# Kernel tuning notes

Hardware: AMD Instinct MI355X
Metric: run time of the kernel (lower is better)

The kernel has to match this reference:

```python
import jax, jax.numpy as jnp
import numpy as np

N_NODES = 100000
N_EDGES = 1600000
IN_DIM, HID_DIM, N_CLASSES = 128, 64, 40


def spmm(edge_row, edge_col, edge_val, dense):
    # sparse [N,N] @ dense [N,D] via gather + segment-sum over edges
    msgs = edge_val[:, None] * dense[edge_col]            # [E, D]
    return jax.ops.segment_sum(msgs, edge_row, num_segments=N_NODES)


def setup_inputs() -> dict:
    key = jax.random.key(0)
    ks = jax.random.split(key, 8)
    x = jax.random.normal(ks[0], (N_NODES, IN_DIM), dtype=jnp.float32)
    edge_row = jax.random.randint(ks[1], (N_EDGES,), 0, N_NODES, dtype=jnp.int32)
    edge_col = jax.random.randint(ks[2], (N_EDGES,), 0, N_NODES, dtype=jnp.int32)
    edge_val = jax.random.uniform(ks[3], (N_EDGES,), dtype=jnp.float32)
    s1 = 1.0 / np.sqrt(IN_DIM)
    s2 = 1.0 / np.sqrt(HID_DIM)
    W1 = jax.random.normal(ks[4], (IN_DIM, HID_DIM), dtype=jnp.float32) * s1
    b1 = jnp.zeros((HID_DIM,), dtype=jnp.float32)
    W2 = jax.random.normal(ks[5], (HID_DIM, HID_DIM), dtype=jnp.float32) * s2
    b2 = jnp.zeros((HID_DIM,), dtype=jnp.float32)
    Wc = jax.random.normal(ks[6], (HID_DIM, N_CLASSES), dtype=jnp.float32) * s2
    bc = jnp.zeros((N_CLASSES,), dtype=jnp.float32)
    return {"x": x, "edge_row": edge_row, "edge_col": edge_col, "edge_val": edge_val,
            "W1": W1, "b1": b1, "W2": W2, "b2": b2, "Wc": Wc, "bc": bc}


def reference(x, edge_row, edge_col, edge_val, W1, b1, W2, b2, Wc, bc):
    # GCN layer 1: support = xW+b, aggregate, relu  (dropout off in eval)
    h = jax.nn.relu(spmm(edge_row, edge_col, edge_val, x @ W1 + b1))
    # GCN layer 2
    h = spmm(edge_row, edge_col, edge_val, h @ W2 + b2)
    # node classifier + log-softmax
    logits = h @ Wc + bc
    return jax.nn.log_softmax(logits, axis=-1)
```

## Files before the change

### kernel.cpp

```cpp
#include <hip/hip_runtime.h>

#define N_NODES   100000
#define N_EDGES   1600000
#define IN_DIM    128
#define HID_DIM   64
#define N_CLASSES 40

#define NBUCK 782
#define BCAP  2816
#define EPB   6400
#define PBLK  1024
#define G1BLK 1563

typedef __attribute__((ext_vector_type(8))) short bf16x8;
typedef __attribute__((ext_vector_type(4))) float f32x4;

__device__ inline short f2bf(float f) {
    unsigned u = __float_as_uint(f);
    unsigned r = (u + 0x7FFFu + ((u >> 16) & 1u)) >> 16;
    return (short)r;
}
__device__ inline float bflo(unsigned w) { return __uint_as_float(w << 16); }
__device__ inline float bfhi(unsigned w) { return __uint_as_float(w & 0xFFFF0000u); }
__device__ inline float upval(unsigned w) { return __uint_as_float((w >> 17) << 16); }

__global__ __launch_bounds__(256) void prep_weights(const float* __restrict__ W1,
                                                    const float* __restrict__ W2,
                                                    const float* __restrict__ Wc,
                                                    const float* __restrict__ b2,
                                                    short* __restrict__ W1t,
                                                    short* __restrict__ Mt,
                                                    float* __restrict__ bv,
                                                    int* __restrict__ bcnt) {
    for (int i = blockIdx.x * 256 + threadIdx.x; i < IN_DIM * HID_DIM; i += gridDim.x * 256) {
        int n = i >> 7, k = i & 127;
        W1t[i] = f2bf(W1[k * HID_DIM + n]);
    }
    if (blockIdx.x == 7) {
        for (int i = threadIdx.x; i < NBUCK; i += 256) bcnt[i] = 0;
    }
    if (blockIdx.x == 0) {
        for (int idx = threadIdx.x; idx < HID_DIM * HID_DIM; idx += 256) {
            int n = idx >> 6, i = idx & 63;
            float acc = 0.f;
            if (n < N_CLASSES)
                for (int j = 0; j < HID_DIM; ++j)
                    acc = fmaf(W2[i * HID_DIM + j], Wc[j * N_CLASSES + n], acc);
            Mt[n * HID_DIM + i] = f2bf(acc);
        }
        for (int n = threadIdx.x; n < N_CLASSES; n += 256) {
            float acc = 0.f;
            for (int j = 0; j < HID_DIM; ++j)
                acc = fmaf(b2[j], Wc[j * N_CLASSES + n], acc);
            bv[n] = acc;
        }
    }
}

__global__ __launch_bounds__(PBLK) void part_a(const int* __restrict__ erow,
                                               const int* __restrict__ ecol,
                                               const float* __restrict__ eval,
                                               int* __restrict__ bcnt,
                                               int2* __restrict__ tmp) {
    __shared__ int2 pay[EPB];
    __shared__ int hist[NBUCK], lbase[NBUCK], cur[NBUCK], dofs[NBUCK], scan[NBUCK];
    int e0 = blockIdx.x * EPB;
    int tid = threadIdx.x;
    for (int i = tid; i < NBUCK; i += PBLK) { hist[i] = 0; cur[i] = 0; }
    __syncthreads();
    for (int i = tid; i < EPB; i += PBLK)
        atomicAdd(&hist[erow[e0 + i] >> 7], 1);
    __syncthreads();
    for (int i = tid; i < NBUCK; i += PBLK) {
        int n = hist[i];
        dofs[i] = i * BCAP + (n ? atomicAdd(&bcnt[i], n) : 0);
        scan[i] = n;
    }
    __syncthreads();
    for (int off = 1; off < NBUCK; off <<= 1) {
        int t = 0;
        if (tid < NBUCK && tid >= off) t = scan[tid - off];
        __syncthreads();
        if (tid < NBUCK) scan[tid] += t;
        __syncthreads();
    }
    if (tid < NBUCK) {
        lbase[tid] = scan[tid] - hist[tid];
        dofs[tid] -= lbase[tid];
    }
    __syncthreads();
    for (int i = tid; i < EPB; i += PBLK) {
        int e = e0 + i;
        int r = erow[e];
        int b = r >> 7;
        int p = lbase[b] + atomicAdd(&cur[b], 1);
        unsigned u = __float_as_uint(eval[e]);
        unsigned vb = ((u + 0x7FFFu + ((u >> 16) & 1u)) >> 16) & 0x7FFFu;
        pay[p] = make_int2(((r & 127) << 17) | ecol[e], (int)((vb << 10) | (unsigned)b));
    }
    __syncthreads();
    for (int p = tid; p < EPB; p += PBLK) {
        int2 v = pay[p];
        int b = (unsigned)v.y & 1023u;
        int dest = dofs[b] + p;
        if (dest < (b + 1) * BCAP)
            tmp[dest] = v;
    }
}

__global__ __launch_bounds__(256) void part_b_gemm1(const int* __restrict__ bcnt,
                                                    const int2* __restrict__ tmp,
                                                    unsigned* __restrict__ tmp2,
                                                    int2* __restrict__ rowmeta,
                                                    const float* __restrict__ x,
                                                    const short* __restrict__ W1t,
                                                    const float* __restrict__ b1,
                                                    unsigned short* __restrict__ outH) {
    __shared__ int2 ein[BCAP];
    __shared__ unsigned eout[BCAP];
    __shared__ int hist[128], pad[128], basep[128], cur[128], scan[128];
    if (blockIdx.x < NBUCK) {
        int b = blockIdx.x;
        int nb = bcnt[b]; if (nb > BCAP) nb = BCAP;
        for (int i = threadIdx.x; i < nb; i += 256) ein[i] = tmp[(size_t)b * BCAP + i];
        if (threadIdx.x < 128) { hist[threadIdx.x] = 0; cur[threadIdx.x] = 0; }
        __syncthreads();
        for (int i = threadIdx.x; i < nb; i += 256)
            atomicAdd(&hist[(ein[i].x >> 17) & 127], 1);
        __syncthreads();
        if (threadIdx.x < 128) {
            pad[threadIdx.x] = (hist[threadIdx.x] + 3) & ~3;
            scan[threadIdx.x] = pad[threadIdx.x];
        }
        __syncthreads();
        for (int off = 1; off < 128; off <<= 1) {
            int t = 0;
            if (threadIdx.x < 128 && threadIdx.x >= off) t = scan[threadIdx.x - off];
            __syncthreads();
            if (threadIdx.x < 128) scan[threadIdx.x] += t;
            __syncthreads();
        }
        if (threadIdx.x < 128) basep[threadIdx.x] = scan[threadIdx.x] - pad[threadIdx.x];
        __syncthreads();
        int ntot = scan[127]; if (ntot > BCAP) ntot = BCAP;
        for (int i = threadIdx.x; i < nb; i += 256) {
            int lr = (ein[i].x >> 17) & 127;
            int p = basep[lr] + atomicAdd(&cur[lr], 1);
            if (p < BCAP) {
                unsigned vb = ((unsigned)ein[i].y >> 10) & 0x7FFFu;
                eout[p] = (vb << 17) | (unsigned)(ein[i].x & 0x1FFFF);
            }
        }
        __syncthreads();
        if (threadIdx.x < 128) {
            int pe = basep[threadIdx.x] + pad[threadIdx.x];
            for (int p = basep[threadIdx.x] + hist[threadIdx.x]; p < pe && p < BCAP; ++p)
                eout[p] = 0u;
        }
        __syncthreads();
        for (int i = threadIdx.x; i < ntot; i += 256) tmp2[(size_t)b * BCAP + i] = eout[i];
        if (threadIdx.x < 128) {
            int r = b * 128 + threadIdx.x;
            if (r < N_NODES)
                rowmeta[r] = make_int2(b * BCAP + basep[threadIdx.x], pad[threadIdx.x]);
        }
    } else {
        int gb = blockIdx.x - NBUCK;
        int wave = threadIdx.x >> 6;
        int lane = threadIdx.x & 63;
        int node0 = gb * 64 + wave * 16;
        if (node0 >= N_NODES) return;
        int m = lane & 15;
        int q = lane >> 4;
        const float* xrow = x + (size_t)(node0 + m) * IN_DIM;
        f32x4 acc0 = {0,0,0,0}, acc1 = {0,0,0,0}, acc2 = {0,0,0,0}, acc3 = {0,0,0,0};
#pragma unroll
        for (int kb = 0; kb < 4; ++kb) {
            int k0 = kb * 32 + q * 8;
            float4 a0 = *(const float4*)(xrow + k0);
            float4 a1 = *(const float4*)(xrow + k0 + 4);
            bf16x8 af;
            af[0]=f2bf(a0.x); af[1]=f2bf(a0.y); af[2]=f2bf(a0.z); af[3]=f2bf(a0.w);
            af[4]=f2bf(a1.x); af[5]=f2bf(a1.y); af[6]=f2bf(a1.z); af[7]=f2bf(a1.w);
            bf16x8 bf0 = *(const bf16x8*)(W1t + ( 0 + m) * IN_DIM + k0);
            bf16x8 bf1 = *(const bf16x8*)(W1t + (16 + m) * IN_DIM + k0);
            bf16x8 bf2 = *(const bf16x8*)(W1t + (32 + m) * IN_DIM + k0);
            bf16x8 bf3 = *(const bf16x8*)(W1t + (48 + m) * IN_DIM + k0);
            acc0 = __builtin_amdgcn_mfma_f32_16x16x32_bf16(af, bf0, acc0, 0, 0, 0);
            acc1 = __builtin_amdgcn_mfma_f32_16x16x32_bf16(af, bf1, acc1, 0, 0, 0);
            acc2 = __builtin_amdgcn_mfma_f32_16x16x32_bf16(af, bf2, acc2, 0, 0, 0);
            acc3 = __builtin_amdgcn_mfma_f32_16x16x32_bf16(af, bf3, acc3, 0, 0, 0);
        }
        f32x4 accs[4] = {acc0, acc1, acc2, acc3};
#pragma unroll
        for (int t = 0; t < 4; ++t) {
            float bias = b1[t * 16 + m];
#pragma unroll
            for (int r = 0; r < 4; ++r) {
                int node = node0 + q * 4 + r;
                outH[(size_t)node * HID_DIM + t * 16 + m] = (unsigned short)f2bf(accs[t][r] + bias);
            }
        }
    }
}

__global__ __launch_bounds__(256) void gemm2u_mfma(const unsigned short* __restrict__ h,
                                                   const short* __restrict__ Mt,
                                                   unsigned short* __restrict__ out) {
    int wave = threadIdx.x >> 6;
    int lane = threadIdx.x & 63;
    int node0 = blockIdx.x * 64 + wave * 16;
    if (node0 >= N_NODES) return;
    int m = lane & 15;
    int q = lane >> 4;
    const unsigned short* hrow = h + (size_t)(node0 + m) * HID_DIM;
    f32x4 acc0 = {0,0,0,0}, acc1 = {0,0,0,0}, acc2 = {0,0,0,0}, acc3 = {0,0,0,0};
#pragma unroll
    for (int kb = 0; kb < 2; ++kb) {
        int k0 = kb * 32 + q * 8;
        bf16x8 af = *(const bf16x8*)(hrow + k0);
#pragma unroll
        for (int j = 0; j < 8; ++j)
            af[j] = ((unsigned short)af[j] & 0x8000u) ? 0 : af[j];
        bf16x8 bf0 = *(const bf16x8*)(Mt + ( 0 + m) * HID_DIM + k0);
        bf16x8 bf1 = *(const bf16x8*)(Mt + (16 + m) * HID_DIM + k0);
        bf16x8 bf2 = *(const bf16x8*)(Mt + (32 + m) * HID_DIM + k0);
        bf16x8 bf3 = *(const bf16x8*)(Mt + (48 + m) * HID_DIM + k0);
        acc0 = __builtin_amdgcn_mfma_f32_16x16x32_bf16(af, bf0, acc0, 0, 0, 0);
        acc1 = __builtin_amdgcn_mfma_f32_16x16x32_bf16(af, bf1, acc1, 0, 0, 0);
        acc2 = __builtin_amdgcn_mfma_f32_16x16x32_bf16(af, bf2, acc2, 0, 0, 0);
        acc3 = __builtin_amdgcn_mfma_f32_16x16x32_bf16(af, bf3, acc3, 0, 0, 0);
    }
    f32x4 accs[4] = {acc0, acc1, acc2, acc3};
#pragma unroll
    for (int t = 0; t < 4; ++t) {
#pragma unroll
        for (int r = 0; r < 4; ++r) {
            int node = node0 + q * 4 + r;
            out[(size_t)node * HID_DIM + t * 16 + m] = (unsigned short)f2bf(accs[t][r]);
        }
    }
}

__global__ __launch_bounds__(256) void spmm_csr(const int2* __restrict__ rowmeta,
                                                const unsigned* __restrict__ ecv,
                                                const unsigned short* __restrict__ dense,
                                                unsigned short* __restrict__ out) {
    __shared__ unsigned lm[4][8][68];
    int wave = threadIdx.x >> 6;
    int lane = threadIdx.x & 63;
    int s = lane >> 3, dq = lane & 7;
    int r = (blockIdx.x * 4 + wave) * 8 + s;
    int2 meta = rowmeta[r];
    int beg = meta.x, deg = meta.y;
    int degc = deg < 64 ? deg : 64;
    for (int e = dq; e < degc; e += 8)
        lm[wave][s][e] = ecv[beg + e];
    __syncthreads();
    const unsigned* mp = lm[wave][s];
    float a0=0,a1=0,a2=0,a3=0,a4=0,a5=0,a6=0,a7=0;
    if (deg > 0) {
        uint4 w = *(const uint4*)mp;
        for (int e = 0; e < degc; e += 4) {
            uint4 wn = (e + 4 < degc) ? *(const uint4*)(mp + e + 4) : w;
            uint4 g0 = *(const uint4*)(dense + ((size_t)(w.x & 0x1FFFF) << 6) + (dq << 3));
            uint4 g1 = *(const uint4*)(dense + ((size_t)(w.y & 0x1FFFF) << 6) + (dq << 3));
            uint4 g2 = *(const uint4*)(dense + ((size_t)(w.z & 0x1FFFF) << 6) + (dq << 3));
            uint4 g3 = *(const uint4*)(dense + ((size_t)(w.w & 0x1FFFF) << 6) + (dq << 3));
            float v0 = upval(w.x), v1 = upval(w.y), v2 = upval(w.z), v3 = upval(w.w);
            a0=fmaf(v0,bflo(g0.x),a0); a1=fmaf(v0,bfhi(g0.x),a1); a2=fmaf(v0,bflo(g0.y),a2); a3=fmaf(v0,bfhi(g0.y),a3);
            a4=fmaf(v0,bflo(g0.z),a4); a5=fmaf(v0,bfhi(g0.z),a5); a6=fmaf(v0,bflo(g0.w),a6); a7=fmaf(v0,bfhi(g0.w),a7);
            a0=fmaf(v1,bflo(g1.x),a0); a1=fmaf(v1,bfhi(g1.x),a1); a2=fmaf(v1,bflo(g1.y),a2); a3=fmaf(v1,bfhi(g1.y),a3);
            a4=fmaf(v1,bflo(g1.z),a4); a5=fmaf(v1,bfhi(g1.z),a5); a6=fmaf(v1,bflo(g1.w),a6); a7=fmaf(v1,bfhi(g1.w),a7);
            a0=fmaf(v2,bflo(g2.x),a0); a1=fmaf(v2,bfhi(g2.x),a1); a2=fmaf(v2,bflo(g2.y),a2); a3=fmaf(v2,bfhi(g2.y),a3);
            a4=fmaf(v2,bflo(g2.z),a4); a5=fmaf(v2,bfhi(g2.z),a5); a6=fmaf(v2,bflo(g2.w),a6); a7=fmaf(v2,bfhi(g2.w),a7);
            a0=fmaf(v3,bflo(g3.x),a0); a1=fmaf(v3,bfhi(g3.x),a1); a2=fmaf(v3,bflo(g3.y),a2); a3=fmaf(v3,bfhi(g3.y),a3);
            a4=fmaf(v3,bflo(g3.z),a4); a5=fmaf(v3,bfhi(g3.z),a5); a6=fmaf(v3,bflo(g3.w),a6); a7=fmaf(v3,bfhi(g3.w),a7);
            w = wn;
        }
        for (int e = 64; e < deg; ++e) {
            unsigned we = ecv[beg + e];
            uint4 g = *(const uint4*)(dense + ((size_t)(we & 0x1FFFF) << 6) + (dq << 3));
            float v = upval(we);
            a0=fmaf(v,bflo(g.x),a0); a1=fmaf(v,bfhi(g.x),a1); a2=fmaf(v,bflo(g.y),a2); a3=fmaf(v,bfhi(g.y),a3);
            a4=fmaf(v,bflo(g.z),a4); a5=fmaf(v,bfhi(g.z),a5); a6=fmaf(v,bflo(g.w),a6); a7=fmaf(v,bfhi(g.w),a7);
        }
    }
    uint4 o;
    o.x = (unsigned short)f2bf(a0) | ((unsigned)(unsigned short)f2bf(a1) << 16);
    o.y = (unsigned short)f2bf(a2) | ((unsigned)(unsigned short)f2bf(a3) << 16);
    o.z = (unsigned short)f2bf(a4) | ((unsigned)(unsigned short)f2bf(a5) << 16);
    o.w = (unsigned short)f2bf(a6) | ((unsigned)(unsigned short)f2bf(a7) << 16);
    *(uint4*)(out + (size_t)r * HID_DIM + (dq << 3)) = o;
}

__global__ __launch_bounds__(256) void spmm_cls(const int2* __restrict__ rowmeta,
                                                const unsigned* __restrict__ ecv,
                                                const unsigned short* __restrict__ dense,
                                                const float* __restrict__ bv,
                                                const float* __restrict__ bc,
                                                float* __restrict__ outF) {
    __shared__ unsigned lm[4][8][68];
    int wave = threadIdx.x >> 6;
    int lane = threadIdx.x & 63;
    int s = lane >> 3, dq = lane & 7;
    int r = (blockIdx.x * 4 + wave) * 8 + s;
    float4 bv0 = {0,0,0,0}, bv1 = {0,0,0,0}, bc0 = {0,0,0,0}, bc1 = {0,0,0,0};
    if (dq < 5) {
        bv0 = *(const float4*)(bv + dq * 8);  bv1 = *(const float4*)(bv + dq * 8 + 4);
        bc0 = *(const float4*)(bc + dq * 8);  bc1 = *(const float4*)(bc + dq * 8 + 4);
    }
    int2 meta = rowmeta[r];
    int beg = meta.x, deg = meta.y;
    int degc = deg < 64 ? deg : 64;
    for (int e = dq; e < degc; e += 8)
        lm[wave][s][e] = ecv[beg + e];
    __syncthreads();
    const unsigned* mp = lm[wave][s];
    float a0=0,a1=0,a2=0,a3=0,a4=0,a5=0,a6=0,a7=0, asum=0;
    if (deg > 0) {
        uint4 w = *(const uint4*)mp;
        for (int e = 0; e < degc; e += 4) {
            uint4 wn = (e + 4 < degc) ? *(const uint4*)(mp + e + 4) : w;
            uint4 g0 = *(const uint4*)(dense + ((size_t)(w.x & 0x1FFFF) << 6) + (dq << 3));
            uint4 g1 = *(const uint4*)(dense + ((size_t)(w.y & 0x1FFFF) << 6) + (dq << 3));
            uint4 g2 = *(const uint4*)(dense + ((size_t)(w.z & 0x1FFFF) << 6) + (dq << 3));
            uint4 g3 = *(const uint4*)(dense + ((size_t)(w.w & 0x1FFFF) << 6) + (dq << 3));
            float v0 = upval(w.x), v1 = upval(w.y), v2 = upval(w.z), v3 = upval(w.w);
            asum += v0 + v1 + v2 + v3;
            a0=fmaf(v0,bflo(g0.x),a0); a1=fmaf(v0,bfhi(g0.x),a1); a2=fmaf(v0,bflo(g0.y),a2); a3=fmaf(v0,bfhi(g0.y),a3);
            a4=fmaf(v0,bflo(g0.z),a4); a5=fmaf(v0,bfhi(g0.z),a5); a6=fmaf(v0,bflo(g0.w),a6); a7=fmaf(v0,bfhi(g0.w),a7);
            a0=fmaf(v1,bflo(g1.x),a0); a1=fmaf(v1,bfhi(g1.x),a1); a2=fmaf(v1,bflo(g1.y),a2); a3=fmaf(v1,bfhi(g1.y),a3);
            a4=fmaf(v1,bflo(g1.z),a4); a5=fmaf(v1,bfhi(g1.z),a5); a6=fmaf(v1,bflo(g1.w),a6); a7=fmaf(v1,bfhi(g1.w),a7);
            a0=fmaf(v2,bflo(g2.x),a0); a1=fmaf(v2,bfhi(g2.x),a1); a2=fmaf(v2,bflo(g2.y),a2); a3=fmaf(v2,bfhi(g2.y),a3);
            a4=fmaf(v2,bflo(g2.z),a4); a5=fmaf(v2,bfhi(g2.z),a5); a6=fmaf(v2,bflo(g2.w),a6); a7=fmaf(v2,bfhi(g2.w),a7);
            a0=fmaf(v3,bflo(g3.x),a0); a1=fmaf(v3,bfhi(g3.x),a1); a2=fmaf(v3,bflo(g3.y),a2); a3=fmaf(v3,bfhi(g3.y),a3);
            a4=fmaf(v3,bflo(g3.z),a4); a5=fmaf(v3,bfhi(g3.z),a5); a6=fmaf(v3,bflo(g3.w),a6); a7=fmaf(v3,bfhi(g3.w),a7);
            w = wn;
        }
        for (int e = 64; e < deg; ++e) {
            unsigned we = ecv[beg + e];
            uint4 g = *(const uint4*)(dense + ((size_t)(we & 0x1FFFF) << 6) + (dq << 3));
            float v = upval(we);
            asum += v;
            a0=fmaf(v,bflo(g.x),a0); a1=fmaf(v,bfhi(g.x),a1); a2=fmaf(v,bflo(g.y),a2); a3=fmaf(v,bfhi(g.y),a3);
            a4=fmaf(v,bflo(g.z),a4); a5=fmaf(v,bfhi(g.z),a5); a6=fmaf(v,bflo(g.w),a6); a7=fmaf(v,bfhi(g.w),a7);
        }
    }
    float l0 = fmaf(asum, bv0.x, a0) + bc0.x;
    float l1 = fmaf(asum, bv0.y, a1) + bc0.y;
    float l2 = fmaf(asum, bv0.z, a2) + bc0.z;
    float l3 = fmaf(asum, bv0.w, a3) + bc0.w;
    float l4 = fmaf(asum, bv1.x, a4) + bc1.x;
    float l5 = fmaf(asum, bv1.y, a5) + bc1.y;
    float l6 = fmaf(asum, bv1.z, a6) + bc1.z;
    float l7 = fmaf(asum, bv1.w, a7) + bc1.w;
    float mx = -1e30f;
    if (dq < 5)
        mx = fmaxf(fmaxf(fmaxf(l0, l1), fmaxf(l2, l3)),
                   fmaxf(fmaxf(l4, l5), fmaxf(l6, l7)));
#pragma unroll
    for (int off = 1; off < 8; off <<= 1) mx = fmaxf(mx, __shfl_xor(mx, off));
    float ss = 0.f;
    if (dq < 5)
        ss = __expf(l0 - mx) + __expf(l1 - mx) + __expf(l2 - mx) + __expf(l3 - mx)
           + __expf(l4 - mx) + __expf(l5 - mx) + __expf(l6 - mx) + __expf(l7 - mx);
#pragma unroll
    for (int off = 1; off < 8; off <<= 1) ss += __shfl_xor(ss, off);
    float lse = mx + __logf(ss);
    if (dq < 5) {
        float4 o0 = {l0 - lse, l1 - lse, l2 - lse, l3 - lse};
        float4 o1 = {l4 - lse, l5 - lse, l6 - lse, l7 - lse};
        float* dst = outF + (size_t)r * N_CLASSES + dq * 8;
        *(float4*)(dst) = o0;
        *(float4*)(dst + 4) = o1;
    }
}

extern "C" void kernel_launch(void* const* d_in, const int* in_sizes, int n_in,
                              void* d_out, int out_size, void* d_ws, size_t ws_size,
                              hipStream_t stream) {
    const float* x    = (const float*)d_in[0];
    const int*   erow = (const int*)  d_in[1];
    const int*   ecol = (const int*)  d_in[2];
    const float* eval = (const float*)d_in[3];
    const float* W1   = (const float*)d_in[4];
    const float* b1   = (const float*)d_in[5];
    const float* W2   = (const float*)d_in[6];
    const float* b2   = (const float*)d_in[7];
    const float* Wc   = (const float*)d_in[8];
    const float* bc   = (const float*)d_in[9];
    float* out = (float*)d_out;

    char* ws = (char*)d_ws;
    size_t off = 0;
    auto alloc = [&](size_t bytes) { char* p = ws + off; off += (bytes + 255) & ~(size_t)255; return p; };
    unsigned short* bufA = (unsigned short*)alloc((size_t)N_NODES * HID_DIM * sizeof(short));
    unsigned short* bufB = (unsigned short*)alloc((size_t)N_NODES * HID_DIM * sizeof(short));
    int2*     tmp     = (int2*)    alloc((size_t)NBUCK * BCAP * sizeof(int2));
    unsigned* tmp2    = (unsigned*)alloc((size_t)NBUCK * BCAP * sizeof(unsigned));
    int2*     rowmeta = (int2*)    alloc((size_t)N_NODES * sizeof(int2));
    int*      bcnt    = (int*)     alloc(NBUCK * sizeof(int));
    short*    W1t     = (short*)   alloc((size_t)IN_DIM * HID_DIM * sizeof(short));
    short*    Mt      = (short*)   alloc((size_t)HID_DIM * HID_DIM * sizeof(short));
    float*    bv      = (float*)   alloc(64 * sizeof(float));

    const int tile_grid = (N_NODES + 63) / 64;
    const int spmm_grid = N_NODES / 32;
    const int grid_a    = (N_EDGES + EPB - 1) / EPB;

    prep_weights<<<8, 256, 0, stream>>>(W1, W2, Wc, b2, W1t, Mt, bv, bcnt);
    part_a<<<grid_a, PBLK, 0, stream>>>(erow, ecol, eval, bcnt, tmp);
    part_b_gemm1<<<NBUCK + tile_grid, 256, 0, stream>>>(bcnt, tmp, tmp2, rowmeta,
                                                        x, W1t, b1, bufA);
    spmm_csr<<<spmm_grid, 256, 0, stream>>>(rowmeta, tmp2, bufA, bufB);
    gemm2u_mfma<<<tile_grid, 256, 0, stream>>>(bufB, Mt, bufA);
    spmm_cls<<<spmm_grid, 256, 0, stream>>>(rowmeta, tmp2, bufA, bv, bc, out);
}
```

Measured before the change: 262.1 us.

## Fuse weight prep into partition kernel and fuse SpMM1 with the W2·Wc GEMM

The weight-preparation kernel is merged into the edge-partition kernel as extra blocks, and the bucket counters are now zeroed with a memset. The first SpMM now applies ReLU, stages its 32 output rows in swizzled shared memory, and multiplies them by the folded W2·Wc matrix with MFMA in the same kernel. This removes one launch and the bf16 round trip through global memory for the intermediate hidden layer. In exchange the SpMM kernel uses more shared memory and adds a block-wide sync, which may lower occupancy.

```diff
diff --git a/kernel.cpp b/kernel.cpp
--- a/kernel.cpp
+++ b/kernel.cpp
@@ -10,7 +10,7 @@
 #define BCAP  2816
 #define EPB   6400
 #define PBLK  1024
-#define G1BLK 1563
+#define GRID_A 250
 
 typedef __attribute__((ext_vector_type(8))) short bf16x8;
 typedef __attribute__((ext_vector_type(4))) float f32x4;
@@ -24,48 +24,47 @@
 __device__ inline float bfhi(unsigned w) { return __uint_as_float(w & 0xFFFF0000u); }
 __device__ inline float upval(unsigned w) { return __uint_as_float((w >> 17) << 16); }
 
-__global__ __launch_bounds__(256) void prep_weights(const float* __restrict__ W1,
-                                                    const float* __restrict__ W2,
-                                                    const float* __restrict__ Wc,
-                                                    const float* __restrict__ b2,
-                                                    short* __restrict__ W1t,
-                                                    short* __restrict__ Mt,
-                                                    float* __restrict__ bv,
-                                                    int* __restrict__ bcnt) {
-    for (int i = blockIdx.x * 256 + threadIdx.x; i < IN_DIM * HID_DIM; i += gridDim.x * 256) {
-        int n = i >> 7, k = i & 127;
-        W1t[i] = f2bf(W1[k * HID_DIM + n]);
-    }
-    if (blockIdx.x == 7) {
-        for (int i = threadIdx.x; i < NBUCK; i += 256) bcnt[i] = 0;
-    }
-    if (blockIdx.x == 0) {
-        for (int idx = threadIdx.x; idx < HID_DIM * HID_DIM; idx += 256) {
-            int n = idx >> 6, i = idx & 63;
-            float acc = 0.f;
-            if (n < N_CLASSES)
-                for (int j = 0; j < HID_DIM; ++j)
-                    acc = fmaf(W2[i * HID_DIM + j], Wc[j * N_CLASSES + n], acc);
-            Mt[n * HID_DIM + i] = f2bf(acc);
-        }
-        for (int n = threadIdx.x; n < N_CLASSES; n += 256) {
+__global__ __launch_bounds__(PBLK) void prep_parta(const int* __restrict__ erow,
+                                                   const int* __restrict__ ecol,
+                                                   const float* __restrict__ eval,
+                                                   int* __restrict__ bcnt,
+                                                   int2* __restrict__ tmp,
+                                                   const float* __restrict__ W1,
+                                                   const float* __restrict__ W2,
+                                                   const float* __restrict__ Wc,
+                                                   const float* __restrict__ b2,
+                                                   short* __restrict__ W1t,
+                                                   short* __restrict__ Mt,
+                                                   float* __restrict__ bv) {
+    __shared__ int2 pay[EPB];
+    __shared__ int hist[NBUCK], lbase[NBUCK], cur[NBUCK], dofs[NBUCK], scan[NBUCK];
+    int tid = threadIdx.x;
+    if (blockIdx.x >= GRID_A) {
+        int pb = blockIdx.x - GRID_A;
+        {
+            int i = pb * PBLK + tid;
+            int n = i >> 7, k = i & 127;
+            W1t[i] = f2bf(W1[k * HID_DIM + n]);
+        }
+        if (pb == 0) {
+            for (int idx = tid; idx < HID_DIM * HID_DIM; idx += PBLK) {
+                int n = idx >> 6, i = idx & 63;
+                float acc = 0.f;
+                if (n < N_CLASSES)
+                    for (int j = 0; j < HID_DIM; ++j)
+                        acc = fmaf(W2[i * HID_DIM + j], Wc[j * N_CLASSES + n], acc);
+                Mt[n * HID_DIM + i] = f2bf(acc);
+            }
+        }
+        if (pb == 1 && tid < N_CLASSES) {
             float acc = 0.f;
             for (int j = 0; j < HID_DIM; ++j)
-                acc = fmaf(b2[j], Wc[j * N_CLASSES + n], acc);
-            bv[n] = acc;
-        }
-    }
-}
-
-__global__ __launch_bounds__(PBLK) void part_a(const int* __restrict__ erow,
-                                               const int* __restrict__ ecol,
-                                               const float* __restrict__ eval,
-                                               int* __restrict__ bcnt,
-                                               int2* __restrict__ tmp) {
-    __shared__ int2 pay[EPB];
-    __shared__ int hist[NBUCK], lbase[NBUCK], cur[NBUCK], dofs[NBUCK], scan[NBUCK];
+                acc = fmaf(b2[j], Wc[j * N_CLASSES + tid], acc);
+            bv[tid] = acc;
+        }
+        return;
+    }
     int e0 = blockIdx.x * EPB;
-    int tid = threadIdx.x;
     for (int i = tid; i < NBUCK; i += PBLK) { hist[i] = 0; cur[i] = 0; }
     __syncthreads();
     for (int i = tid; i < EPB; i += PBLK)
@@ -204,53 +203,18 @@
     }
 }
 
-__global__ __launch_bounds__(256) void gemm2u_mfma(const unsigned short* __restrict__ h,
-                                                   const short* __restrict__ Mt,
-                                                   unsigned short* __restrict__ out) {
-    int wave = threadIdx.x >> 6;
-    int lane = threadIdx.x & 63;
-    int node0 = blockIdx.x * 64 + wave * 16;
-    if (node0 >= N_NODES) return;
-    int m = lane & 15;
-    int q = lane >> 4;
-    const unsigned short* hrow = h + (size_t)(node0 + m) * HID_DIM;
-    f32x4 acc0 = {0,0,0,0}, acc1 = {0,0,0,0}, acc2 = {0,0,0,0}, acc3 = {0,0,0,0};
-#pragma unroll
-    for (int kb = 0; kb < 2; ++kb) {
-        int k0 = kb * 32 + q * 8;
-        bf16x8 af = *(const bf16x8*)(hrow + k0);
-#pragma unroll
-        for (int j = 0; j < 8; ++j)
-            af[j] = ((unsigned short)af[j] & 0x8000u) ? 0 : af[j];
-        bf16x8 bf0 = *(const bf16x8*)(Mt + ( 0 + m) * HID_DIM + k0);
-        bf16x8 bf1 = *(const bf16x8*)(Mt + (16 + m) * HID_DIM + k0);
-        bf16x8 bf2 = *(const bf16x8*)(Mt + (32 + m) * HID_DIM + k0);
-        bf16x8 bf3 = *(const bf16x8*)(Mt + (48 + m) * HID_DIM + k0);
-        acc0 = __builtin_amdgcn_mfma_f32_16x16x32_bf16(af, bf0, acc0, 0, 0, 0);
-        acc1 = __builtin_amdgcn_mfma_f32_16x16x32_bf16(af, bf1, acc1, 0, 0, 0);
-        acc2 = __builtin_amdgcn_mfma_f32_16x16x32_bf16(af, bf2, acc2, 0, 0, 0);
-        acc3 = __builtin_amdgcn_mfma_f32_16x16x32_bf16(af, bf3, acc3, 0, 0, 0);
-    }
-    f32x4 accs[4] = {acc0, acc1, acc2, acc3};
-#pragma unroll
-    for (int t = 0; t < 4; ++t) {
-#pragma unroll
-        for (int r = 0; r < 4; ++r) {
-            int node = node0 + q * 4 + r;
-            out[(size_t)node * HID_DIM + t * 16 + m] = (unsigned short)f2bf(accs[t][r]);
-        }
-    }
-}
-
-__global__ __launch_bounds__(256) void spmm_csr(const int2* __restrict__ rowmeta,
+__global__ __launch_bounds__(256) void spmm1_mm(const int2* __restrict__ rowmeta,
                                                 const unsigned* __restrict__ ecv,
                                                 const unsigned short* __restrict__ dense,
-                                                unsigned short* __restrict__ out) {
+                                                const short* __restrict__ Mt,
+                                                unsigned short* __restrict__ outU) {
     __shared__ unsigned lm[4][8][68];
+    __shared__ unsigned short tr[32][64];
     int wave = threadIdx.x >> 6;
     int lane = threadIdx.x & 63;
     int s = lane >> 3, dq = lane & 7;
-    int r = (blockIdx.x * 4 + wave) * 8 + s;
+    int row = wave * 8 + s;
+    int r = blockIdx.x * 32 + row;
     int2 meta = rowmeta[r];
     int beg = meta.x, deg = meta.y;
     int degc = deg < 64 ? deg : 64;
@@ -287,11 +251,34 @@
         }
     }
     uint4 o;
-    o.x = (unsigned short)f2bf(a0) | ((unsigned)(unsigned short)f2bf(a1) << 16);
-    o.y = (unsigned short)f2bf(a2) | ((unsigned)(unsigned short)f2bf(a3) << 16);
-    o.z = (unsigned short)f2bf(a4) | ((unsigned)(unsigned short)f2bf(a5) << 16);
-    o.w = (unsigned short)f2bf(a6) | ((unsigned)(unsigned short)f2bf(a7) << 16);
-    *(uint4*)(out + (size_t)r * HID_DIM + (dq << 3)) = o;
+    o.x = (unsigned short)f2bf(fmaxf(a0,0.f)) | ((unsigned)(unsigned short)f2bf(fmaxf(a1,0.f)) << 16);
+    o.y = (unsigned short)f2bf(fmaxf(a2,0.f)) | ((unsigned)(unsigned short)f2bf(fmaxf(a3,0.f)) << 16);
+    o.z = (unsigned short)f2bf(fmaxf(a4,0.f)) | ((unsigned)(unsigned short)f2bf(fmaxf(a5,0.f)) << 16);
+    o.w = (unsigned short)f2bf(fmaxf(a6,0.f)) | ((unsigned)(unsigned short)f2bf(fmaxf(a7,0.f)) << 16);
+    *(uint4*)(&tr[row][(dq ^ s) << 3]) = o;
+    __syncthreads();
+    int m = lane & 15;
+    int q = lane >> 4;
+    int nt = wave >> 1;
+    int tb = (wave & 1) << 1;
+    int arow = nt * 16 + m;
+    f32x4 c0 = {0,0,0,0}, c1 = {0,0,0,0};
+#pragma unroll
+    for (int kb = 0; kb < 2; ++kb) {
+        int ch = kb * 4 + q;
+        bf16x8 af = *(const bf16x8*)(&tr[arow][(ch ^ (arow & 7)) << 3]);
+        int k0 = kb * 32 + q * 8;
+        bf16x8 bf0 = *(const bf16x8*)(Mt + ((tb + 0) * 16 + m) * HID_DIM + k0);
+        bf16x8 bf1 = *(const bf16x8*)(Mt + ((tb + 1) * 16 + m) * HID_DIM + k0);
+        c0 = __builtin_amdgcn_mfma_f32_16x16x32_bf16(af, bf0, c0, 0, 0, 0);
+        c1 = __builtin_amdgcn_mfma_f32_16x16x32_bf16(af, bf1, c1, 0, 0, 0);
+    }
+#pragma unroll
+    for (int rr = 0; rr < 4; ++rr) {
+        int node = blockIdx.x * 32 + nt * 16 + q * 4 + rr;
+        outU[(size_t)node * HID_DIM + (tb + 0) * 16 + m] = (unsigned short)f2bf(c0[rr]);
+        outU[(size_t)node * HID_DIM + (tb + 1) * 16 + m] = (unsigned short)f2bf(c1[rr]);
+    }
 }
 
 __global__ __launch_bounds__(256) void spmm_cls(const int2* __restrict__ rowmeta,
@@ -407,13 +394,12 @@
 
     const int tile_grid = (N_NODES + 63) / 64;
     const int spmm_grid = N_NODES / 32;
-    const int grid_a    = (N_EDGES + EPB - 1) / EPB;
-
-    prep_weights<<<8, 256, 0, stream>>>(W1, W2, Wc, b2, W1t, Mt, bv, bcnt);
-    part_a<<<grid_a, PBLK, 0, stream>>>(erow, ecol, eval, bcnt, tmp);
+
+    hipMemsetAsync(bcnt, 0, NBUCK * sizeof(int), stream);
+    prep_parta<<<GRID_A + 8, PBLK, 0, stream>>>(erow, ecol, eval, bcnt, tmp,
+                                                W1, W2, Wc, b2, W1t, Mt, bv);
     part_b_gemm1<<<NBUCK + tile_grid, 256, 0, stream>>>(bcnt, tmp, tmp2, rowmeta,
                                                         x, W1t, b1, bufA);
-    spmm_csr<<<spmm_grid, 256, 0, stream>>>(rowmeta, tmp2, bufA, bufB);
-    gemm2u_mfma<<<tile_grid, 256, 0, stream>>>(bufB, Mt, bufA);
-    spmm_cls<<<spmm_grid, 256, 0, stream>>>(rowmeta, tmp2, bufA, bv, bc, out);
-}
+    spmm1_mm<<<spmm_grid, 256, 0, stream>>>(rowmeta, tmp2, bufA, Mt, bufB);
+    spmm_cls<<<spmm_grid, 256, 0, stream>>>(rowmeta, tmp2, bufB, bv, bc, out);
+}
```

Result: faster. 232.3 us (-11.4%).
